# Performance work log

Measured on AMD Instinct MI355X. Metric: run time of the kernel, lower is better.

## Reference

```python
import jax, jax.numpy as jnp
import numpy as np

NUM_SCENES = 7
SHAPE = [512, 512, 256, 64]  # layer dims: 512->512->256->64
BATCH = 16384


def _xavier(key, shape):
    # nn.init.xavier_normal_ on (s, in, out): fan_in/fan_out from last two dims
    fan_in, fan_out = shape[-2], shape[-1]
    std = np.sqrt(2.0 / (fan_in + fan_out)).astype(np.float32)
    return jax.random.normal(key, shape, dtype=jnp.float32) * std


def setup_inputs() -> dict:
    key = jax.random.key(0)
    ks = jax.random.split(key, 16)
    inp = {
        "x": jax.random.normal(ks[0], (BATCH, SHAPE[0]), dtype=jnp.float32),
        "scene": jax.random.randint(ks[1], (BATCH,), 1, NUM_SCENES + 1, dtype=jnp.int64),
    }
    for i in range(3):
        din, dout = SHAPE[i], SHAPE[i + 1]
        inp[f"W{i}"] = _xavier(ks[2 + 4 * i], (NUM_SCENES, din, dout))
        inp[f"b{i}"] = jnp.zeros((NUM_SCENES, dout), dtype=jnp.float32)
        inp[f"gW{i}"] = _xavier(ks[3 + 4 * i], (1, din, dout))
        inp[f"gb{i}"] = jnp.zeros((1, dout), dtype=jnp.float32)
    return inp


def _star_linear(x, scene0, W, b, gW, gb, relu):
    # W: (S, in, out), gW: (1, in, out). Equivalent to gathering W[scene0]
    # and doing x[:,None,:] @ (w * gW), but computed as a dense GEMM over
    # all scenes followed by a per-sample select (avoids B*in*out gather).
    scaled = W * gW                                   # (S, in, out)
    out_all = jnp.einsum('bi,sio->bso', x, scaled)    # (B, S, out)
    out = jnp.take_along_axis(out_all, scene0[:, None, None], axis=1)[:, 0, :]
    out = out + b[scene0] + gb[0]
    if relu:
        out = jnp.maximum(out, 0.0)
    return out  # dropout is identity at eval


def reference(x, scene, W0, b0, gW0, gb0, W1, b1, gW1, gb1, W2, b2, gW2, gb2):
    scene0 = (scene - 1).astype(jnp.int32)
    h = _star_linear(x, scene0, W0, b0, gW0, gb0, relu=True)
    h = _star_linear(h, scene0, W1, b1, gW1, gb1, relu=True)
    h = _star_linear(h, scene0, W2, b2, gW2, gb2, relu=False)  # drop=True -> no relu
    return h
```

## Files before the change

kernel.cpp:

```cpp
#include <hip/hip_runtime.h>
#include <hip/hip_bf16.h>
#include <stdint.h>


#define BATCH   16384
#define NSCENE  7
#define TM      128
#define NBLK    (BATCH / 256)
#define MT_MAX  (BATCH / TM + NSCENE)
#define PADMAX  (BATCH + NSCENE * TM)

typedef __bf16 bf16x8 __attribute__((ext_vector_type(8)));
typedef float  f32x4  __attribute__((ext_vector_type(4)));

__device__ __forceinline__ ushort f2bf(float f) {
  union { float f; uint32_t u; } v; v.f = f;
  uint32_t r = (v.u + 0x7FFFu + ((v.u >> 16) & 1u)) >> 16;
  return (ushort)r;
}
__device__ __forceinline__ uint32_t pk2(float a, float b) {
  union { __hip_bfloat162 h; uint32_t u; } cv;
  cv.h = __float22bfloat162_rn(make_float2(a, b));
  return cv.u;
}
__device__ __forceinline__ void async16(const void* g, void* lds) {
  __builtin_amdgcn_global_load_lds(
      (const __attribute__((address_space(1))) uint32_t*)g,
      (__attribute__((address_space(3))) uint32_t*)lds, 16, 0, 0);
}

__device__ __forceinline__ void st_tile(const float* __restrict__ W,
                                        const float* __restrict__ gW,
                                        ushort* __restrict__ sT,
                                        int K, int N, int s, int n0, int k0,
                                        int tid) {
  __shared__ float tl[32][33];
  int tx = tid & 31, ty = tid >> 5;
  const float* Wp = W + (size_t)s * K * N;
#pragma unroll
  for (int i = 0; i < 4; i++) {
    int k = k0 + ty + i * 8;
    tl[ty + i * 8][tx] = Wp[(size_t)k * N + n0 + tx] * gW[(size_t)k * N + n0 + tx];
  }
  __syncthreads();
#pragma unroll
  for (int i = 0; i < 4; i++) {
    int n = n0 + ty + i * 8;
    sT[((size_t)s * N + n) * K + k0 + tx] = f2bf(tl[tx][ty + i * 8]);
  }
}

#define NB_W0 (16 * 16 * 7)
#define NB_W1 (8 * 16 * 7)
#define NB_W2 (2 * 8 * 7)
#define NB_BIAS 23
#define NB_CNT NBLK

__global__ __launch_bounds__(256) void prep_k(
    const float* __restrict__ W0, const float* __restrict__ gW0,
    const float* __restrict__ W1, const float* __restrict__ gW1,
    const float* __restrict__ W2, const float* __restrict__ gW2,
    const float* __restrict__ b0, const float* __restrict__ gb0,
    const float* __restrict__ b1, const float* __restrict__ gb1,
    const float* __restrict__ b2, const float* __restrict__ gb2,
    const int* __restrict__ scene,
    ushort* __restrict__ sT0, ushort* __restrict__ sT1, ushort* __restrict__ sT2,
    float* __restrict__ bias0, float* __restrict__ bias1, float* __restrict__ bias2,
    int* __restrict__ bcnt, int* __restrict__ rank) {
  int bid = blockIdx.x, tid = threadIdx.x;
  if (bid < NB_W0) {
    int l = bid;
    st_tile(W0, gW0, sT0, 512, 512, l / 256, (l % 16) * 32, ((l / 16) % 16) * 32, tid);
  } else if (bid < NB_W0 + NB_W1) {
    int l = bid - NB_W0;
    st_tile(W1, gW1, sT1, 512, 256, l / 128, (l % 8) * 32, ((l / 8) % 16) * 32, tid);
  } else if (bid < NB_W0 + NB_W1 + NB_W2) {
    int l = bid - NB_W0 - NB_W1;
    st_tile(W2, gW2, sT2, 256, 64, l / 16, (l % 2) * 32, ((l / 2) % 8) * 32, tid);
  } else if (bid < NB_W0 + NB_W1 + NB_W2 + NB_BIAS) {
    int t = (bid - NB_W0 - NB_W1 - NB_W2) * 256 + tid;
    if (t < 7 * 512) bias0[t] = b0[t] + gb0[t & 511];
    else if (t < 7 * 512 + 7 * 256) { int i = t - 7 * 512; bias1[i] = b1[i] + gb1[i & 255]; }
    else if (t < 7 * 512 + 7 * 256 + 7 * 64) { int i = t - 7 * 512 - 7 * 256; bias2[i] = b2[i] + gb2[i & 63]; }
  } else {
    __shared__ int l[NSCENE];
    if (tid < NSCENE) l[tid] = 0;
    __syncthreads();
    int blk = bid - NB_W0 - NB_W1 - NB_W2 - NB_BIAS;
    int i = blk * 256 + tid;
    int pos = atomicAdd(&l[scene[i] - 1], 1);
    rank[i] = pos;
    __syncthreads();
    if (tid < NSCENE) bcnt[blk * NSCENE + tid] = l[tid];
  }
}

#define PLAN_SHARED  __shared__ int sb[NBLK * NSCENE]; \
                     __shared__ int tot[NSCENE], padoff[NSCENE], cumt[NSCENE + 1];
__device__ __forceinline__ void plan_derive(const int* __restrict__ bcnt,
                                            int* sb, int* tot, int* padoff,
                                            int* cumt, int tid) {
  if (tid < NBLK * NSCENE) sb[tid] = bcnt[tid];
  if (tid + 256 < NBLK * NSCENE) sb[tid + 256] = bcnt[tid + 256];
  __syncthreads();
  if (tid < NSCENE) {
    int c = 0;
    for (int b = 0; b < NBLK; b++) c += sb[b * NSCENE + tid];
    tot[tid] = c;
  }
  __syncthreads();
  if (tid == 0) {
    int po = 0, ct = 0;
    for (int s = 0; s < NSCENE; s++) {
      padoff[s] = po; cumt[s] = ct;
      int tiles = (tot[s] + TM - 1) / TM;
      ct += tiles; po += tiles * TM;
    }
    cumt[NSCENE] = ct;
  }
  __syncthreads();
}

__global__ __launch_bounds__(256) void xc_k(const float* __restrict__ x,
                                            const int* __restrict__ scene,
                                            const int* __restrict__ rank,
                                            const int* __restrict__ bcnt,
                                            int* __restrict__ idxp,
                                            ushort* __restrict__ xc) {
  PLAN_SHARED
  __shared__ int base7[NSCENE];
  int tid = threadIdx.x;
  plan_derive(bcnt, sb, tot, padoff, cumt, tid);
  int myblk = blockIdx.x >> 5;
  if (tid < NSCENE) {
    int pre = 0;
    for (int b = 0; b < myblk; b++) pre += sb[b * NSCENE + tid];
    base7[tid] = padoff[tid] + pre;
  }
  __syncthreads();

  int r = blockIdx.x * 8 + (tid >> 5);
  int s = scene[r] - 1;
  int d = base7[s] + rank[r];
  if ((tid & 31) == 0) idxp[d] = r;
  int c = (tid & 31) * 16;
  const float4* p = (const float4*)(x + (size_t)r * 512 + c);
  float4 f0 = p[0], f1 = p[1], f2 = p[2], f3 = p[3];
  uint4 v0, v1;
  v0.x = pk2(f0.x, f0.y); v0.y = pk2(f0.z, f0.w);
  v0.z = pk2(f1.x, f1.y); v0.w = pk2(f1.z, f1.w);
  v1.x = pk2(f2.x, f2.y); v1.y = pk2(f2.z, f2.w);
  v1.z = pk2(f3.x, f3.y); v1.w = pk2(f3.z, f3.w);
  uint4* q = (uint4*)(xc + (size_t)d * 512 + c);
  q[0] = v0; q[1] = v1;
}

__global__ __launch_bounds__(256) void gemm0_k(
    const ushort* __restrict__ ain, const ushort* __restrict__ bw,
    const float* __restrict__ bias, const int* __restrict__ bcnt,
    ushort* __restrict__ hout) {
  PLAN_SHARED
  __shared__ __align__(16) ushort Abuf[64 * 64];
  __shared__ __align__(16) ushort Bbuf[128 * 64];

  int tid = threadIdx.x;
  plan_derive(bcnt, sb, tot, padoff, cumt, tid);

  int j = blockIdx.x;
  int t = j >> 1;
  if (t >= cumt[NSCENE]) return;
  int sc = 0;
  while (sc < NSCENE - 1 && t >= cumt[sc + 1]) sc++;
  int mrow0 = padoff[sc] + (t - cumt[sc]) * TM + (j & 1) * 64;
  int nb = blockIdx.y;

  int lane = tid & 63, wid = tid >> 6;

  f32x4 acc[4][2];
#pragma unroll
  for (int mt = 0; mt < 4; mt++)
#pragma unroll
    for (int nt = 0; nt < 2; nt++) acc[mt][nt] = (f32x4){0.f, 0.f, 0.f, 0.f};

  const ushort* bwS = bw + ((size_t)sc * 512 + (size_t)nb * 128) * 512;

  for (int kb = 0; kb < 8; kb++) {
#pragma unroll
    for (int i = 0; i < 2; i++) {
      int c = tid + i * 256;
      int row = c >> 3, q = c & 7;
      int kg = q ^ (row & 7);
      async16(ain + (size_t)(mrow0 + row) * 512 + kb * 64 + kg * 8,
              &Abuf[(size_t)(i * 256 + wid * 64) * 8]);
    }
#pragma unroll
    for (int i = 0; i < 4; i++) {
      int c = tid + i * 256;
      int row = c >> 3, q = c & 7;
      int kg = q ^ (row & 7);
      async16(bwS + (size_t)row * 512 + kb * 64 + kg * 8,
              &Bbuf[(size_t)(i * 256 + wid * 64) * 8]);
    }
    __syncthreads();
#pragma unroll
    for (int kk = 0; kk < 64; kk += 32) {
      bf16x8 af[4], bfr[2];
      int kc = (kk >> 3) + (lane >> 4);
#pragma unroll
      for (int mt = 0; mt < 4; mt++) {
        int row = mt * 16 + (lane & 15);
        af[mt] = *(const bf16x8*)(&Abuf[(row * 8 + (kc ^ (row & 7))) * 8]);
      }
#pragma unroll
      for (int nt = 0; nt < 2; nt++) {
        int row = wid * 32 + nt * 16 + (lane & 15);
        bfr[nt] = *(const bf16x8*)(&Bbuf[(row * 8 + (kc ^ (row & 7))) * 8]);
      }
#pragma unroll
      for (int mt = 0; mt < 4; mt++)
#pragma unroll
        for (int nt = 0; nt < 2; nt++)
          acc[mt][nt] = __builtin_amdgcn_mfma_f32_16x16x32_bf16(af[mt], bfr[nt], acc[mt][nt], 0, 0, 0);
    }
    __syncthreads();
  }

#pragma unroll
  for (int mt = 0; mt < 4; mt++) {
    int rl0 = mt * 16 + (lane >> 4) * 4;
#pragma unroll
    for (int nt = 0; nt < 2; nt++) {
      int col = nb * 128 + wid * 32 + nt * 16 + (lane & 15);
      float bv = bias[sc * 512 + col];
#pragma unroll
      for (int r = 0; r < 4; r++) {
        float v = fmaxf(acc[mt][nt][r] + bv, 0.f);
        hout[(size_t)(mrow0 + rl0 + r) * 512 + col] = f2bf(v);
      }
    }
  }
}

__global__ __launch_bounds__(256) void gemm12_k(
    const ushort* __restrict__ hc1, const ushort* __restrict__ sT1,
    const ushort* __restrict__ sT2, const float* __restrict__ bias1,
    const float* __restrict__ bias2, const int* __restrict__ bcnt,
    const int* __restrict__ idxp, float* __restrict__ out) {
  PLAN_SHARED
  __shared__ __align__(16) ushort Abuf[64 * 64];
  __shared__ __align__(16) ushort Bbuf[256 * 64];
  __shared__ __align__(16) ushort h2[64 * 256];

  int tid = threadIdx.x;
  plan_derive(bcnt, sb, tot, padoff, cumt, tid);

  int j = blockIdx.x;
  int t = j >> 1;
  if (t >= cumt[NSCENE]) return;
  int sc = 0;
  while (sc < NSCENE - 1 && t >= cumt[sc + 1]) sc++;
  int mrow0 = padoff[sc] + (t - cumt[sc]) * TM + (j & 1) * 64;
  int maxloc = padoff[sc] + tot[sc];

  int lane = tid & 63, wid = tid >> 6;

  f32x4 acc[4][4];
#pragma unroll
  for (int mt = 0; mt < 4; mt++)
#pragma unroll
    for (int nt = 0; nt < 4; nt++) acc[mt][nt] = (f32x4){0.f, 0.f, 0.f, 0.f};

  const ushort* b1p = sT1 + (size_t)sc * 256 * 512;

  for (int kb = 0; kb < 8; kb++) {
#pragma unroll
    for (int i = 0; i < 2; i++) {
      int c = tid + i * 256;
      int row = c >> 3, q = c & 7;
      int kg = q ^ (row & 7);
      async16(hc1 + (size_t)(mrow0 + row) * 512 + kb * 64 + kg * 8,
              &Abuf[(size_t)(i * 256 + wid * 64) * 8]);
    }
#pragma unroll
    for (int i = 0; i < 8; i++) {
      int c = tid + i * 256;
      int row = c >> 3, q = c & 7;
      int kg = q ^ (row & 7);
      async16(b1p + (size_t)row * 512 + kb * 64 + kg * 8,
              &Bbuf[(size_t)(i * 256 + wid * 64) * 8]);
    }
    __syncthreads();
#pragma unroll
    for (int kk = 0; kk < 64; kk += 32) {
      bf16x8 af[4], bfr[4];
      int kc = (kk >> 3) + (lane >> 4);
#pragma unroll
      for (int mt = 0; mt < 4; mt++) {
        int row = mt * 16 + (lane & 15);
        af[mt] = *(const bf16x8*)(&Abuf[(row * 8 + (kc ^ (row & 7))) * 8]);
      }
#pragma unroll
      for (int nt = 0; nt < 4; nt++) {
        int row = wid * 64 + nt * 16 + (lane & 15);
        bfr[nt] = *(const bf16x8*)(&Bbuf[(row * 8 + (kc ^ (row & 7))) * 8]);
      }
#pragma unroll
      for (int mt = 0; mt < 4; mt++)
#pragma unroll
        for (int nt = 0; nt < 4; nt++)
          acc[mt][nt] = __builtin_amdgcn_mfma_f32_16x16x32_bf16(af[mt], bfr[nt], acc[mt][nt], 0, 0, 0);
    }
    __syncthreads();
  }

#pragma unroll
  for (int mt = 0; mt < 4; mt++) {
#pragma unroll
    for (int nt = 0; nt < 4; nt++) {
      int col = wid * 64 + nt * 16 + (lane & 15);
      float bv = bias1[sc * 256 + col];
#pragma unroll
      for (int r = 0; r < 4; r++) {
        int row = mt * 16 + (lane >> 4) * 4 + r;
        float v = fmaxf(acc[mt][nt][r] + bv, 0.f);
        h2[(row * 32 + ((col >> 3) ^ (row & 7))) * 8 + (col & 7)] = f2bf(v);
      }
    }
  }

  const ushort* b2p = sT2 + (size_t)sc * 64 * 256;
#pragma unroll
  for (int i = 0; i < 8; i++) {
    int p = tid + i * 256;
    int row = p >> 5, pc = p & 31;
    int kg = pc ^ (row & 7);
    async16(b2p + (size_t)row * 256 + kg * 8,
            &Bbuf[(size_t)(i * 256 + wid * 64) * 8]);
  }
  __syncthreads();

  f32x4 acc2[4];
#pragma unroll
  for (int nt = 0; nt < 4; nt++) acc2[nt] = (f32x4){0.f, 0.f, 0.f, 0.f};

#pragma unroll
  for (int kk = 0; kk < 256; kk += 32) {
    int kf = (kk >> 3) + (lane >> 4);
    bf16x8 af;
    {
      int row = wid * 16 + (lane & 15);
      af = *(const bf16x8*)(&h2[(row * 32 + (kf ^ (row & 7))) * 8]);
    }
    bf16x8 bfr[4];
#pragma unroll
    for (int nt = 0; nt < 4; nt++) {
      int n = nt * 16 + (lane & 15);
      bfr[nt] = *(const bf16x8*)(&Bbuf[(n * 32 + (kf ^ (n & 7))) * 8]);
    }
#pragma unroll
    for (int nt = 0; nt < 4; nt++)
      acc2[nt] = __builtin_amdgcn_mfma_f32_16x16x32_bf16(af, bfr[nt], acc2[nt], 0, 0, 0);
  }

  int rowg[4], gidx[4];
#pragma unroll
  for (int r = 0; r < 4; r++) {
    rowg[r] = mrow0 + wid * 16 + (lane >> 4) * 4 + r;
    gidx[r] = idxp[rowg[r]];
  }
#pragma unroll
  for (int nt = 0; nt < 4; nt++) {
    int col = nt * 16 + (lane & 15);
    float bv = bias2[sc * 64 + col];
#pragma unroll
    for (int r = 0; r < 4; r++) {
      if (rowg[r] < maxloc) out[(size_t)gidx[r] * 64 + col] = acc2[nt][r] + bv;
    }
  }
}

extern "C" void kernel_launch(void* const* d_in, const int* in_sizes, int n_in,
                              void* d_out, int out_size, void* d_ws, size_t ws_size,
                              hipStream_t stream) {
  const float* x   = (const float*)d_in[0];
  const int* scene = (const int*)d_in[1];
  const float* W0  = (const float*)d_in[2];
  const float* b0  = (const float*)d_in[3];
  const float* gW0 = (const float*)d_in[4];
  const float* gb0 = (const float*)d_in[5];
  const float* W1  = (const float*)d_in[6];
  const float* b1  = (const float*)d_in[7];
  const float* gW1 = (const float*)d_in[8];
  const float* gb1 = (const float*)d_in[9];
  const float* W2  = (const float*)d_in[10];
  const float* b2  = (const float*)d_in[11];
  const float* gW2 = (const float*)d_in[12];
  const float* gb2 = (const float*)d_in[13];
  float* out = (float*)d_out;

  char* ws = (char*)d_ws;
  size_t off = 0;
  auto alloc = [&](size_t bytes) -> void* {
    void* p = ws + off;
    off = (off + bytes + 255) & ~(size_t)255;
    return p;
  };
  ushort* sT0   = (ushort*)alloc((size_t)7 * 512 * 512 * 2);
  ushort* sT1   = (ushort*)alloc((size_t)7 * 256 * 512 * 2);
  ushort* sT2   = (ushort*)alloc((size_t)7 * 64 * 256 * 2);
  float*  bias0 = (float*)alloc(7 * 512 * 4);
  float*  bias1 = (float*)alloc(7 * 256 * 4);
  float*  bias2 = (float*)alloc(7 * 64 * 4);
  int*    bcnt  = (int*)alloc(NBLK * NSCENE * 4);
  int*    rank  = (int*)alloc(BATCH * 4);
  int*    idxp  = (int*)alloc(PADMAX * 4);
  ushort* xc    = (ushort*)alloc((size_t)PADMAX * 512 * 2);
  ushort* hc1   = (ushort*)alloc((size_t)PADMAX * 512 * 2);
  (void)ws_size; (void)n_in; (void)in_sizes; (void)out_size;

  prep_k<<<NB_W0 + NB_W1 + NB_W2 + NB_BIAS + NB_CNT, 256, 0, stream>>>(
      W0, gW0, W1, gW1, W2, gW2, b0, gb0, b1, gb1, b2, gb2, scene,
      sT0, sT1, sT2, bias0, bias1, bias2, bcnt, rank);
  xc_k<<<BATCH / 8, 256, 0, stream>>>(x, scene, rank, bcnt, idxp, xc);

  gemm0_k<<<dim3(MT_MAX * 2, 4), 256, 0, stream>>>(xc, sT0, bias0, bcnt, hc1);
  gemm12_k<<<dim3(MT_MAX * 2), 256, 0, stream>>>(hc1, sT1, sT2, bias1, bias2,
                                                 bcnt, idxp, out);
}
```

Measured before the change: 152.2 us.

## Double-buffer fused layer-1/2 GEMM with 512 threads and precomputed plan

The xc_k kernel now writes the scene plan (counts, padded offsets, cumulative tiles) to global memory once. The two GEMM kernels read that plan instead of each block re-deriving it from the per-block counts. The fused layer-1/2 kernel moves to 512 threads with double-buffered A/B shared tiles, prefetches the layer-2 weights during the last K step, and skips tiles that are entirely padding. This is meant to cut per-block plan overhead and hide global-load latency, at the cost of more shared memory (about 112KB), which may limit occupancy.

Result: slower. 159.9 us (+5.0%).

```diff
diff --git a/kernel.cpp b/kernel.cpp
--- a/kernel.cpp
+++ b/kernel.cpp
@@ -126,11 +126,16 @@
                                             const int* __restrict__ rank,
                                             const int* __restrict__ bcnt,
                                             int* __restrict__ idxp,
-                                            ushort* __restrict__ xc) {
+                                            ushort* __restrict__ xc,
+                                            int* __restrict__ plan_g) {
   PLAN_SHARED
   __shared__ int base7[NSCENE];
   int tid = threadIdx.x;
   plan_derive(bcnt, sb, tot, padoff, cumt, tid);
+  if (blockIdx.x == 0) {
+    if (tid < NSCENE) { plan_g[tid] = tot[tid]; plan_g[7 + tid] = padoff[tid]; }
+    if (tid < NSCENE + 1) plan_g[14 + tid] = cumt[tid];
+  }
   int myblk = blockIdx.x >> 5;
   if (tid < NSCENE) {
     int pre = 0;
@@ -157,14 +162,17 @@
 
 __global__ __launch_bounds__(256) void gemm0_k(
     const ushort* __restrict__ ain, const ushort* __restrict__ bw,
-    const float* __restrict__ bias, const int* __restrict__ bcnt,
+    const float* __restrict__ bias, const int* __restrict__ plan,
     ushort* __restrict__ hout) {
-  PLAN_SHARED
+  __shared__ int splan[24];
   __shared__ __align__(16) ushort Abuf[64 * 64];
   __shared__ __align__(16) ushort Bbuf[128 * 64];
 
   int tid = threadIdx.x;
-  plan_derive(bcnt, sb, tot, padoff, cumt, tid);
+  if (tid < 22) splan[tid] = plan[tid];
+  __syncthreads();
+  const int* padoff = splan + 7;
+  const int* cumt   = splan + 14;
 
   int j = blockIdx.x;
   int t = j >> 1;
@@ -241,18 +249,52 @@
   }
 }
 
-__global__ __launch_bounds__(256) void gemm12_k(
+__device__ __forceinline__ void stage_ab12(const ushort* __restrict__ ain,
+                                           const ushort* __restrict__ bw,
+                                           ushort* Ab, ushort* Bb,
+                                           int mrow0, int kb, int tid, int wid) {
+  {
+    int c = tid, row = c >> 3, q = c & 7;
+    int kg = q ^ (row & 7);
+    async16(ain + (size_t)(mrow0 + row) * 512 + kb * 64 + kg * 8,
+            Ab + (size_t)(wid * 64) * 8);
+  }
+#pragma unroll
+  for (int i = 0; i < 4; i++) {
+    int c = tid + i * 512, row = c >> 3, q = c & 7;
+    int kg = q ^ (row & 7);
+    async16(bw + (size_t)row * 512 + kb * 64 + kg * 8,
+            Bb + (size_t)(i * 512 + wid * 64) * 8);
+  }
+}
+__device__ __forceinline__ void stage_b2f(const ushort* __restrict__ b2p,
+                                          ushort* Bb, int tid, int wid) {
+#pragma unroll
+  for (int i = 0; i < 4; i++) {
+    int p = tid + i * 512, row = p >> 5, pc = p & 31;
+    int kg = pc ^ (row & 7);
+    async16(b2p + (size_t)row * 256 + kg * 8,
+            Bb + (size_t)(i * 512 + wid * 64) * 8);
+  }
+}
+
+__global__ __launch_bounds__(512, 2) void gemm12_k(
     const ushort* __restrict__ hc1, const ushort* __restrict__ sT1,
     const ushort* __restrict__ sT2, const float* __restrict__ bias1,
-    const float* __restrict__ bias2, const int* __restrict__ bcnt,
+    const float* __restrict__ bias2, const int* __restrict__ plan,
     const int* __restrict__ idxp, float* __restrict__ out) {
-  PLAN_SHARED
-  __shared__ __align__(16) ushort Abuf[64 * 64];
-  __shared__ __align__(16) ushort Bbuf[256 * 64];
+  __shared__ int splan[24];
+  __shared__ __align__(16) ushort Abuf[2][64 * 64];
+  __shared__ __align__(16) ushort Bbuf[2][256 * 64];
+  __shared__ __align__(16) ushort B2buf[64 * 256];
   __shared__ __align__(16) ushort h2[64 * 256];
 
   int tid = threadIdx.x;
-  plan_derive(bcnt, sb, tot, padoff, cumt, tid);
+  if (tid < 22) splan[tid] = plan[tid];
+  __syncthreads();
+  const int* tot    = splan;
+  const int* padoff = splan + 7;
+  const int* cumt   = splan + 14;
 
   int j = blockIdx.x;
   int t = j >> 1;
@@ -261,53 +303,48 @@
   while (sc < NSCENE - 1 && t >= cumt[sc + 1]) sc++;
   int mrow0 = padoff[sc] + (t - cumt[sc]) * TM + (j & 1) * 64;
   int maxloc = padoff[sc] + tot[sc];
+  if (mrow0 >= maxloc) return;
 
   int lane = tid & 63, wid = tid >> 6;
 
-  f32x4 acc[4][4];
+  const ushort* b1p = sT1 + (size_t)sc * 256 * 512;
+  const ushort* b2p = sT2 + (size_t)sc * 64 * 256;
+
+  f32x4 acc[4][2];
 #pragma unroll
   for (int mt = 0; mt < 4; mt++)
 #pragma unroll
-    for (int nt = 0; nt < 4; nt++) acc[mt][nt] = (f32x4){0.f, 0.f, 0.f, 0.f};
-
-  const ushort* b1p = sT1 + (size_t)sc * 256 * 512;
+    for (int nt = 0; nt < 2; nt++) acc[mt][nt] = (f32x4){0.f, 0.f, 0.f, 0.f};
+
+  stage_ab12(hc1, b1p, Abuf[0], Bbuf[0], mrow0, 0, tid, wid);
+  __syncthreads();
 
   for (int kb = 0; kb < 8; kb++) {
-#pragma unroll
-    for (int i = 0; i < 2; i++) {
-      int c = tid + i * 256;
-      int row = c >> 3, q = c & 7;
-      int kg = q ^ (row & 7);
-      async16(hc1 + (size_t)(mrow0 + row) * 512 + kb * 64 + kg * 8,
-              &Abuf[(size_t)(i * 256 + wid * 64) * 8]);
-    }
-#pragma unroll
-    for (int i = 0; i < 8; i++) {
-      int c = tid + i * 256;
-      int row = c >> 3, q = c & 7;
-      int kg = q ^ (row & 7);
-      async16(b1p + (size_t)row * 512 + kb * 64 + kg * 8,
-              &Bbuf[(size_t)(i * 256 + wid * 64) * 8]);
-    }
-    __syncthreads();
+    const ushort* Ac = Abuf[kb & 1];
+    const ushort* Bc = Bbuf[kb & 1];
+    if (kb < 7)
+      stage_ab12(hc1, b1p, Abuf[(kb & 1) ^ 1], Bbuf[(kb & 1) ^ 1],
+                 mrow0, kb + 1, tid, wid);
+    else
+      stage_b2f(b2p, B2buf, tid, wid);
 #pragma unroll
     for (int kk = 0; kk < 64; kk += 32) {
-      bf16x8 af[4], bfr[4];
+      bf16x8 af[4], bfr[2];
       int kc = (kk >> 3) + (lane >> 4);
 #pragma unroll
       for (int mt = 0; mt < 4; mt++) {
         int row = mt * 16 + (lane & 15);
-        af[mt] = *(const bf16x8*)(&Abuf[(row * 8 + (kc ^ (row & 7))) * 8]);
-      }
-#pragma unroll
-      for (int nt = 0; nt < 4; nt++) {
-        int row = wid * 64 + nt * 16 + (lane & 15);
-        bfr[nt] = *(const bf16x8*)(&Bbuf[(row * 8 + (kc ^ (row & 7))) * 8]);
+        af[mt] = *(const bf16x8*)(&Ac[(row * 8 + (kc ^ (row & 7))) * 8]);
+      }
+#pragma unroll
+      for (int nt = 0; nt < 2; nt++) {
+        int row = wid * 32 + nt * 16 + (lane & 15);
+        bfr[nt] = *(const bf16x8*)(&Bc[(row * 8 + (kc ^ (row & 7))) * 8]);
       }
 #pragma unroll
       for (int mt = 0; mt < 4; mt++)
 #pragma unroll
-        for (int nt = 0; nt < 4; nt++)
+        for (int nt = 0; nt < 2; nt++)
           acc[mt][nt] = __builtin_amdgcn_mfma_f32_16x16x32_bf16(af[mt], bfr[nt], acc[mt][nt], 0, 0, 0);
     }
     __syncthreads();
@@ -316,8 +353,8 @@
 #pragma unroll
   for (int mt = 0; mt < 4; mt++) {
 #pragma unroll
-    for (int nt = 0; nt < 4; nt++) {
-      int col = wid * 64 + nt * 16 + (lane & 15);
+    for (int nt = 0; nt < 2; nt++) {
+      int col = wid * 32 + nt * 16 + (lane & 15);
       float bv = bias1[sc * 256 + col];
 #pragma unroll
       for (int r = 0; r < 4; r++) {
@@ -327,50 +364,38 @@
       }
     }
   }
-
-  const ushort* b2p = sT2 + (size_t)sc * 64 * 256;
-#pragma unroll
-  for (int i = 0; i < 8; i++) {
-    int p = tid + i * 256;
-    int row = p >> 5, pc = p & 31;
-    int kg = pc ^ (row & 7);
-    async16(b2p + (size_t)row * 256 + kg * 8,
-            &Bbuf[(size_t)(i * 256 + wid * 64) * 8]);
-  }
-  __syncthreads();
-
-  f32x4 acc2[4];
-#pragma unroll
-  for (int nt = 0; nt < 4; nt++) acc2[nt] = (f32x4){0.f, 0.f, 0.f, 0.f};
-
+  __syncthreads();
+
+  f32x4 acc2[2];
+  acc2[0] = (f32x4){0.f, 0.f, 0.f, 0.f};
+  acc2[1] = (f32x4){0.f, 0.f, 0.f, 0.f};
+  int rbase = (wid >> 1) * 16;
+  int cbase = (wid & 1) * 32;
 #pragma unroll
   for (int kk = 0; kk < 256; kk += 32) {
     int kf = (kk >> 3) + (lane >> 4);
-    bf16x8 af;
-    {
-      int row = wid * 16 + (lane & 15);
-      af = *(const bf16x8*)(&h2[(row * 32 + (kf ^ (row & 7))) * 8]);
-    }
-    bf16x8 bfr[4];
-#pragma unroll
-    for (int nt = 0; nt < 4; nt++) {
-      int n = nt * 16 + (lane & 15);
-      bfr[nt] = *(const bf16x8*)(&Bbuf[(n * 32 + (kf ^ (n & 7))) * 8]);
-    }
-#pragma unroll
-    for (int nt = 0; nt < 4; nt++)
+    int arow = rbase + (lane & 15);
+    bf16x8 af = *(const bf16x8*)(&h2[(arow * 32 + (kf ^ (arow & 7))) * 8]);
+    bf16x8 bfr[2];
+#pragma unroll
+    for (int nt = 0; nt < 2; nt++) {
+      int n = cbase + nt * 16 + (lane & 15);
+      bfr[nt] = *(const bf16x8*)(&B2buf[(n * 32 + (kf ^ (n & 7))) * 8]);
+    }
+#pragma unroll
+    for (int nt = 0; nt < 2; nt++)
       acc2[nt] = __builtin_amdgcn_mfma_f32_16x16x32_bf16(af, bfr[nt], acc2[nt], 0, 0, 0);
   }
 
   int rowg[4], gidx[4];
 #pragma unroll
   for (int r = 0; r < 4; r++) {
-    rowg[r] = mrow0 + wid * 16 + (lane >> 4) * 4 + r;
+    rowg[r] = mrow0 + rbase + (lane >> 4) * 4 + r;
     gidx[r] = idxp[rowg[r]];
   }
 #pragma unroll
-  for (int nt = 0; nt < 4; nt++) {
-    int col = nt * 16 + (lane & 15);
+  for (int nt = 0; nt < 2; nt++) {
+    int col = cbase + nt * 16 + (lane & 15);
     float bv = bias2[sc * 64 + col];
 #pragma unroll
     for (int r = 0; r < 4; r++) {
@@ -414,6 +439,7 @@
   int*    bcnt  = (int*)alloc(NBLK * NSCENE * 4);
   int*    rank  = (int*)alloc(BATCH * 4);
   int*    idxp  = (int*)alloc(PADMAX * 4);
+  int*    plan  = (int*)alloc(32 * 4);
   ushort* xc    = (ushort*)alloc((size_t)PADMAX * 512 * 2);
   ushort* hc1   = (ushort*)alloc((size_t)PADMAX * 512 * 2);
   (void)ws_size; (void)n_in; (void)in_sizes; (void)out_size;
@@ -421,9 +447,9 @@
   prep_k<<<NB_W0 + NB_W1 + NB_W2 + NB_BIAS + NB_CNT, 256, 0, stream>>>(
       W0, gW0, W1, gW1, W2, gW2, b0, gb0, b1, gb1, b2, gb2, scene,
       sT0, sT1, sT2, bias0, bias1, bias2, bcnt, rank);
-  xc_k<<<BATCH / 8, 256, 0, stream>>>(x, scene, rank, bcnt, idxp, xc);
-
-  gemm0_k<<<dim3(MT_MAX * 2, 4), 256, 0, stream>>>(xc, sT0, bias0, bcnt, hc1);
-  gemm12_k<<<dim3(MT_MAX * 2), 256, 0, stream>>>(hc1, sT1, sT2, bias1, bias2,
-                                                 bcnt, idxp, out);
-}
+  xc_k<<<BATCH / 8, 256, 0, stream>>>(x, scene, rank, bcnt, idxp, xc, plan);
+
+  gemm0_k<<<dim3(MT_MAX * 2, 4), 256, 0, stream>>>(xc, sT0, bias0, plan, hc1);
+  gemm12_k<<<dim3(MT_MAX * 2), 512, 0, stream>>>(hc1, sT1, sT2, bias1, bias2,
+                                                 plan, idxp, out);
+}
```

## Fuse input gather and bf16 conversion into first GEMM, precompute plan once

Applied to the files above, without the earlier changes.

Removes the separate pass that gathered x rows into scene-sorted order and converted them to bf16. The first GEMM now reads fp32 x rows directly through an index array and converts to bf16 while filling shared memory, which avoids writing and re-reading an intermediate buffer. A small index kernel writes the scene plan to global memory once, so the GEMMs no longer recompute it per block, and it zeroes the padding indices. The second GEMM also exits early on tiles made entirely of padding. The trade-off is that A-tile loads become synchronous gathers with in-register conversion, and x is re-read by each of the four N-blocks.

Result: slower. 156.0 us (+2.5%).

```diff
diff --git a/kernel.cpp b/kernel.cpp
--- a/kernel.cpp
+++ b/kernel.cpp
@@ -121,50 +121,49 @@
   __syncthreads();
 }
 
-__global__ __launch_bounds__(256) void xc_k(const float* __restrict__ x,
-                                            const int* __restrict__ scene,
-                                            const int* __restrict__ rank,
-                                            const int* __restrict__ bcnt,
-                                            int* __restrict__ idxp,
-                                            ushort* __restrict__ xc) {
+__global__ __launch_bounds__(256) void idx_k(const int* __restrict__ scene,
+                                             const int* __restrict__ rank,
+                                             const int* __restrict__ bcnt,
+                                             int* __restrict__ idxp,
+                                             int* __restrict__ plan_g) {
   PLAN_SHARED
   __shared__ int base7[NSCENE];
   int tid = threadIdx.x;
   plan_derive(bcnt, sb, tot, padoff, cumt, tid);
-  int myblk = blockIdx.x >> 5;
+  int myblk = blockIdx.x;
   if (tid < NSCENE) {
     int pre = 0;
     for (int b = 0; b < myblk; b++) pre += sb[b * NSCENE + tid];
     base7[tid] = padoff[tid] + pre;
   }
   __syncthreads();
-
-  int r = blockIdx.x * 8 + (tid >> 5);
-  int s = scene[r] - 1;
-  int d = base7[s] + rank[r];
-  if ((tid & 31) == 0) idxp[d] = r;
-  int c = (tid & 31) * 16;
-  const float4* p = (const float4*)(x + (size_t)r * 512 + c);
-  float4 f0 = p[0], f1 = p[1], f2 = p[2], f3 = p[3];
-  uint4 v0, v1;
-  v0.x = pk2(f0.x, f0.y); v0.y = pk2(f0.z, f0.w);
-  v0.z = pk2(f1.x, f1.y); v0.w = pk2(f1.z, f1.w);
-  v1.x = pk2(f2.x, f2.y); v1.y = pk2(f2.z, f2.w);
-  v1.z = pk2(f3.x, f3.y); v1.w = pk2(f3.z, f3.w);
-  uint4* q = (uint4*)(xc + (size_t)d * 512 + c);
-  q[0] = v0; q[1] = v1;
+  int r = myblk * 256 + tid;
+  idxp[base7[scene[r] - 1] + rank[r]] = r;
+  if (myblk == 0) {
+    if (tid < NSCENE) { plan_g[tid] = tot[tid]; plan_g[7 + tid] = padoff[tid]; }
+    if (tid < NSCENE + 1) plan_g[14 + tid] = cumt[tid];
+    for (int s = 0; s < NSCENE; s++) {
+      int lo = padoff[s] + tot[s];
+      int hi = (s + 1 < NSCENE) ? padoff[s + 1] : cumt[NSCENE] * TM;
+      for (int i = lo + tid; i < hi; i += 256) idxp[i] = 0;
+    }
+  }
 }
 
 __global__ __launch_bounds__(256) void gemm0_k(
-    const ushort* __restrict__ ain, const ushort* __restrict__ bw,
-    const float* __restrict__ bias, const int* __restrict__ bcnt,
-    ushort* __restrict__ hout) {
-  PLAN_SHARED
+    const float* __restrict__ x, const int* __restrict__ idxp,
+    const ushort* __restrict__ bw, const float* __restrict__ bias,
+    const int* __restrict__ plan, ushort* __restrict__ hout) {
+  __shared__ int splan[24];
+  __shared__ int sidx[64];
   __shared__ __align__(16) ushort Abuf[64 * 64];
   __shared__ __align__(16) ushort Bbuf[128 * 64];
 
   int tid = threadIdx.x;
-  plan_derive(bcnt, sb, tot, padoff, cumt, tid);
+  if (tid < 22) splan[tid] = plan[tid];
+  __syncthreads();
+  const int* padoff = splan + 7;
+  const int* cumt   = splan + 14;
 
   int j = blockIdx.x;
   int t = j >> 1;
@@ -174,7 +173,14 @@
   int mrow0 = padoff[sc] + (t - cumt[sc]) * TM + (j & 1) * 64;
   int nb = blockIdx.y;
 
+  if (tid < 64) sidx[tid] = idxp[mrow0 + tid];
+  __syncthreads();
+
   int lane = tid & 63, wid = tid >> 6;
+  int arow = tid >> 2, aq = tid & 3;
+  const float* xp = x + (size_t)sidx[arow] * 512 + aq * 16;
+  ushort* awr0 = &Abuf[((size_t)arow * 8 + ((2 * aq) ^ (arow & 7))) * 8];
+  ushort* awr1 = &Abuf[((size_t)arow * 8 + ((2 * aq + 1) ^ (arow & 7))) * 8];
 
   f32x4 acc[4][2];
 #pragma unroll
@@ -185,14 +191,6 @@
   const ushort* bwS = bw + ((size_t)sc * 512 + (size_t)nb * 128) * 512;
 
   for (int kb = 0; kb < 8; kb++) {
-#pragma unroll
-    for (int i = 0; i < 2; i++) {
-      int c = tid + i * 256;
-      int row = c >> 3, q = c & 7;
-      int kg = q ^ (row & 7);
-      async16(ain + (size_t)(mrow0 + row) * 512 + kb * 64 + kg * 8,
-              &Abuf[(size_t)(i * 256 + wid * 64) * 8]);
-    }
 #pragma unroll
     for (int i = 0; i < 4; i++) {
       int c = tid + i * 256;
@@ -201,6 +199,17 @@
       async16(bwS + (size_t)row * 512 + kb * 64 + kg * 8,
               &Bbuf[(size_t)(i * 256 + wid * 64) * 8]);
     }
+    {
+      const float4* ap = (const float4*)(xp + kb * 64);
+      float4 f0 = ap[0], f1 = ap[1], f2 = ap[2], f3 = ap[3];
+      uint4 u0, u1;
+      u0.x = pk2(f0.x, f0.y); u0.y = pk2(f0.z, f0.w);
+      u0.z = pk2(f1.x, f1.y); u0.w = pk2(f1.z, f1.w);
+      u1.x = pk2(f2.x, f2.y); u1.y = pk2(f2.z, f2.w);
+      u1.z = pk2(f3.x, f3.y); u1.w = pk2(f3.z, f3.w);
+      *(uint4*)awr0 = u0;
+      *(uint4*)awr1 = u1;
+    }
     __syncthreads();
 #pragma unroll
     for (int kk = 0; kk < 64; kk += 32) {
@@ -244,15 +253,19 @@
 __global__ __launch_bounds__(256) void gemm12_k(
     const ushort* __restrict__ hc1, const ushort* __restrict__ sT1,
     const ushort* __restrict__ sT2, const float* __restrict__ bias1,
-    const float* __restrict__ bias2, const int* __restrict__ bcnt,
+    const float* __restrict__ bias2, const int* __restrict__ plan,
     const int* __restrict__ idxp, float* __restrict__ out) {
-  PLAN_SHARED
+  __shared__ int splan[24];
   __shared__ __align__(16) ushort Abuf[64 * 64];
   __shared__ __align__(16) ushort Bbuf[256 * 64];
   __shared__ __align__(16) ushort h2[64 * 256];
 
   int tid = threadIdx.x;
-  plan_derive(bcnt, sb, tot, padoff, cumt, tid);
+  if (tid < 22) splan[tid] = plan[tid];
+  __syncthreads();
+  const int* tot    = splan;
+  const int* padoff = splan + 7;
+  const int* cumt   = splan + 14;
 
   int j = blockIdx.x;
   int t = j >> 1;
@@ -261,6 +274,7 @@
   while (sc < NSCENE - 1 && t >= cumt[sc + 1]) sc++;
   int mrow0 = padoff[sc] + (t - cumt[sc]) * TM + (j & 1) * 64;
   int maxloc = padoff[sc] + tot[sc];
+  if (mrow0 >= maxloc) return;
 
   int lane = tid & 63, wid = tid >> 6;
 
@@ -414,16 +428,16 @@
   int*    bcnt  = (int*)alloc(NBLK * NSCENE * 4);
   int*    rank  = (int*)alloc(BATCH * 4);
   int*    idxp  = (int*)alloc(PADMAX * 4);
-  ushort* xc    = (ushort*)alloc((size_t)PADMAX * 512 * 2);
+  int*    plan  = (int*)alloc(32 * 4);
   ushort* hc1   = (ushort*)alloc((size_t)PADMAX * 512 * 2);
   (void)ws_size; (void)n_in; (void)in_sizes; (void)out_size;
 
   prep_k<<<NB_W0 + NB_W1 + NB_W2 + NB_BIAS + NB_CNT, 256, 0, stream>>>(
       W0, gW0, W1, gW1, W2, gW2, b0, gb0, b1, gb1, b2, gb2, scene,
       sT0, sT1, sT2, bias0, bias1, bias2, bcnt, rank);
-  xc_k<<<BATCH / 8, 256, 0, stream>>>(x, scene, rank, bcnt, idxp, xc);
-
-  gemm0_k<<<dim3(MT_MAX * 2, 4), 256, 0, stream>>>(xc, sT0, bias0, bcnt, hc1);
+  idx_k<<<NBLK, 256, 0, stream>>>(scene, rank, bcnt, idxp, plan);
+
+  gemm0_k<<<dim3(MT_MAX * 2, 4), 256, 0, stream>>>(x, idxp, sT0, bias0, plan, hc1);
   gemm12_k<<<dim3(MT_MAX * 2), 256, 0, stream>>>(hc1, sT1, sT2, bias1, bias2,
-                                                 bcnt, idxp, out);
-}
+                                                 plan, idxp, out);
+}
```

## Enlarge gemm0 tile to 128x128, precompute plan once, skip empty gemm12 tiles

Applied to the files above, without the earlier changes.

gemm0 now has each block compute a full 128x128 output tile using a 2x2 wave layout with 4x4 MFMA accumulators per wave. This halves the block count and raises operand reuse per LDS load. The per-block plan derivation from bcnt is replaced by a 22-int plan that xc_k writes once and the GEMM kernels read into shared memory. gemm12 blocks whose 64-row half lies entirely in padding now exit early. The trade-off is more accumulator registers, which may lower occupancy, and fewer gemm0 blocks for the GPU to spread across CUs.

After: 156.6 us. 1.03x slower.

```diff
diff --git a/kernel.cpp b/kernel.cpp
--- a/kernel.cpp
+++ b/kernel.cpp
@@ -126,11 +126,16 @@
                                             const int* __restrict__ rank,
                                             const int* __restrict__ bcnt,
                                             int* __restrict__ idxp,
-                                            ushort* __restrict__ xc) {
+                                            ushort* __restrict__ xc,
+                                            int* __restrict__ plan_g) {
   PLAN_SHARED
   __shared__ int base7[NSCENE];
   int tid = threadIdx.x;
   plan_derive(bcnt, sb, tot, padoff, cumt, tid);
+  if (blockIdx.x == 0) {
+    if (tid < NSCENE) { plan_g[tid] = tot[tid]; plan_g[7 + tid] = padoff[tid]; }
+    if (tid < NSCENE + 1) plan_g[14 + tid] = cumt[tid];
+  }
   int myblk = blockIdx.x >> 5;
   if (tid < NSCENE) {
     int pre = 0;
@@ -157,36 +162,39 @@
 
 __global__ __launch_bounds__(256) void gemm0_k(
     const ushort* __restrict__ ain, const ushort* __restrict__ bw,
-    const float* __restrict__ bias, const int* __restrict__ bcnt,
+    const float* __restrict__ bias, const int* __restrict__ plan,
     ushort* __restrict__ hout) {
-  PLAN_SHARED
-  __shared__ __align__(16) ushort Abuf[64 * 64];
+  __shared__ int splan[24];
+  __shared__ __align__(16) ushort Abuf[128 * 64];
   __shared__ __align__(16) ushort Bbuf[128 * 64];
 
   int tid = threadIdx.x;
-  plan_derive(bcnt, sb, tot, padoff, cumt, tid);
-
-  int j = blockIdx.x;
-  int t = j >> 1;
+  if (tid < 22) splan[tid] = plan[tid];
+  __syncthreads();
+  const int* padoff = splan + 7;
+  const int* cumt   = splan + 14;
+
+  int t = blockIdx.x;
   if (t >= cumt[NSCENE]) return;
   int sc = 0;
   while (sc < NSCENE - 1 && t >= cumt[sc + 1]) sc++;
-  int mrow0 = padoff[sc] + (t - cumt[sc]) * TM + (j & 1) * 64;
+  int mrow0 = padoff[sc] + (t - cumt[sc]) * TM;
   int nb = blockIdx.y;
 
   int lane = tid & 63, wid = tid >> 6;
-
-  f32x4 acc[4][2];
+  int wr = wid >> 1, wc = wid & 1;
+
+  f32x4 acc[4][4];
 #pragma unroll
   for (int mt = 0; mt < 4; mt++)
 #pragma unroll
-    for (int nt = 0; nt < 2; nt++) acc[mt][nt] = (f32x4){0.f, 0.f, 0.f, 0.f};
+    for (int nt = 0; nt < 4; nt++) acc[mt][nt] = (f32x4){0.f, 0.f, 0.f, 0.f};
 
   const ushort* bwS = bw + ((size_t)sc * 512 + (size_t)nb * 128) * 512;
 
   for (int kb = 0; kb < 8; kb++) {
 #pragma unroll
-    for (int i = 0; i < 2; i++) {
+    for (int i = 0; i < 4; i++) {
       int c = tid + i * 256;
       int row = c >> 3, q = c & 7;
       int kg = q ^ (row & 7);
@@ -204,22 +212,22 @@
     __syncthreads();
 #pragma unroll
     for (int kk = 0; kk < 64; kk += 32) {
-      bf16x8 af[4], bfr[2];
+      bf16x8 af[4], bfr[4];
       int kc = (kk >> 3) + (lane >> 4);
 #pragma unroll
       for (int mt = 0; mt < 4; mt++) {
-        int row = mt * 16 + (lane & 15);
+        int row = wr * 64 + mt * 16 + (lane & 15);
         af[mt] = *(const bf16x8*)(&Abuf[(row * 8 + (kc ^ (row & 7))) * 8]);
       }
 #pragma unroll
-      for (int nt = 0; nt < 2; nt++) {
-        int row = wid * 32 + nt * 16 + (lane & 15);
+      for (int nt = 0; nt < 4; nt++) {
+        int row = wc * 64 + nt * 16 + (lane & 15);
         bfr[nt] = *(const bf16x8*)(&Bbuf[(row * 8 + (kc ^ (row & 7))) * 8]);
       }
 #pragma unroll
       for (int mt = 0; mt < 4; mt++)
 #pragma unroll
-        for (int nt = 0; nt < 2; nt++)
+        for (int nt = 0; nt < 4; nt++)
           acc[mt][nt] = __builtin_amdgcn_mfma_f32_16x16x32_bf16(af[mt], bfr[nt], acc[mt][nt], 0, 0, 0);
     }
     __syncthreads();
@@ -227,10 +235,10 @@
 
 #pragma unroll
   for (int mt = 0; mt < 4; mt++) {
-    int rl0 = mt * 16 + (lane >> 4) * 4;
-#pragma unroll
-    for (int nt = 0; nt < 2; nt++) {
-      int col = nb * 128 + wid * 32 + nt * 16 + (lane & 15);
+    int rl0 = wr * 64 + mt * 16 + (lane >> 4) * 4;
+#pragma unroll
+    for (int nt = 0; nt < 4; nt++) {
+      int col = nb * 128 + wc * 64 + nt * 16 + (lane & 15);
       float bv = bias[sc * 512 + col];
 #pragma unroll
       for (int r = 0; r < 4; r++) {
@@ -244,15 +252,19 @@
 __global__ __launch_bounds__(256) void gemm12_k(
     const ushort* __restrict__ hc1, const ushort* __restrict__ sT1,
     const ushort* __restrict__ sT2, const float* __restrict__ bias1,
-    const float* __restrict__ bias2, const int* __restrict__ bcnt,
+    const float* __restrict__ bias2, const int* __restrict__ plan,
     const int* __restrict__ idxp, float* __restrict__ out) {
-  PLAN_SHARED
+  __shared__ int splan[24];
   __shared__ __align__(16) ushort Abuf[64 * 64];
   __shared__ __align__(16) ushort Bbuf[256 * 64];
   __shared__ __align__(16) ushort h2[64 * 256];
 
   int tid = threadIdx.x;
-  plan_derive(bcnt, sb, tot, padoff, cumt, tid);
+  if (tid < 22) splan[tid] = plan[tid];
+  __syncthreads();
+  const int* tot    = splan;
+  const int* padoff = splan + 7;
+  const int* cumt   = splan + 14;
 
   int j = blockIdx.x;
   int t = j >> 1;
@@ -261,6 +273,7 @@
   while (sc < NSCENE - 1 && t >= cumt[sc + 1]) sc++;
   int mrow0 = padoff[sc] + (t - cumt[sc]) * TM + (j & 1) * 64;
   int maxloc = padoff[sc] + tot[sc];
+  if (mrow0 >= maxloc) return;
 
   int lane = tid & 63, wid = tid >> 6;
 
@@ -414,6 +427,7 @@
   int*    bcnt  = (int*)alloc(NBLK * NSCENE * 4);
   int*    rank  = (int*)alloc(BATCH * 4);
   int*    idxp  = (int*)alloc(PADMAX * 4);
+  int*    plan  = (int*)alloc(32 * 4);
   ushort* xc    = (ushort*)alloc((size_t)PADMAX * 512 * 2);
   ushort* hc1   = (ushort*)alloc((size_t)PADMAX * 512 * 2);
   (void)ws_size; (void)n_in; (void)in_sizes; (void)out_size;
@@ -421,9 +435,9 @@
   prep_k<<<NB_W0 + NB_W1 + NB_W2 + NB_BIAS + NB_CNT, 256, 0, stream>>>(
       W0, gW0, W1, gW1, W2, gW2, b0, gb0, b1, gb1, b2, gb2, scene,
       sT0, sT1, sT2, bias0, bias1, bias2, bcnt, rank);
-  xc_k<<<BATCH / 8, 256, 0, stream>>>(x, scene, rank, bcnt, idxp, xc);
-
-  gemm0_k<<<dim3(MT_MAX * 2, 4), 256, 0, stream>>>(xc, sT0, bias0, bcnt, hc1);
+  xc_k<<<BATCH / 8, 256, 0, stream>>>(x, scene, rank, bcnt, idxp, xc, plan);
+
+  gemm0_k<<<dim3(MT_MAX, 4), 256, 0, stream>>>(xc, sT0, bias0, plan, hc1);
   gemm12_k<<<dim3(MT_MAX * 2), 256, 0, stream>>>(hc1, sT1, sT2, bias1, bias2,
-                                                 bcnt, idxp, out);
-}
+                                                 plan, idxp, out);
+}
```
